# Performance work log

Measured on AMD Instinct MI355X. Metric: run time of the kernel, lower is better.

Reference implementation:

```python
import jax, jax.numpy as jnp
import numpy as np

B, N, D, E, H, F, L = 4096, 32, 128, 256, 8, 1024, 6
DH = E // H  # head dim = 32
LN_EPS = 1e-5


def setup_inputs() -> dict:
    key = jax.random.key(0)
    ks = jax.random.split(key, 8)
    def s(k, shape, fan_in):
        return (jax.random.normal(k, shape, jnp.float32) / np.float32(np.sqrt(fan_in)))
    inp = {
        "obs": jax.random.normal(ks[0], (B, D), jnp.float32),
        "emb_W": s(ks[1], (N, D, E), D),          # per-node tokenizer Linear weights
        "emb_b": jnp.zeros((N, E), jnp.float32),
        "pos_emb": jax.random.normal(ks[2], (N, E), jnp.float32) * 0.02,
        "Wqkv": s(ks[3], (3 * E, E), E),          # shared across all L layers (torch code shares one layer object)
        "bqkv": jnp.zeros((3 * E,), jnp.float32),
        "Wo": s(ks[4], (E, E), E),
        "bo": jnp.zeros((E,), jnp.float32),
        "ln1_g": jnp.ones((E,), jnp.float32),
        "ln1_b": jnp.zeros((E,), jnp.float32),
        "ln2_g": jnp.ones((E,), jnp.float32),
        "ln2_b": jnp.zeros((E,), jnp.float32),
        "W1": s(ks[5], (E, F), E),
        "b1": jnp.zeros((F,), jnp.float32),
        "W2": s(ks[6], (F, E), F),
        "b2": jnp.zeros((E,), jnp.float32),
    }
    # kinematic-chain adjacency (|i-j|<=1) incl. forced self-loops, additive mask
    idx = jnp.arange(N)
    adj = jnp.abs(idx[:, None] - idx[None, :]) <= 1
    inp["adj_mask"] = jnp.where(adj, 0.0, -1e9).astype(jnp.float32)  # [N, N]
    return inp


def _layer_norm(x, g, b):
    m = jnp.mean(x, axis=-1, keepdims=True)
    v = jnp.var(x, axis=-1, keepdims=True)
    return (x - m) * jax.lax.rsqrt(v + LN_EPS) * g + b


def _encoder_layer(x, adj_mask, Wqkv, bqkv, Wo, bo, ln1_g, ln1_b, ln2_g, ln2_b, W1, b1, W2, b2):
    # pre-LN self-attention block
    h = _layer_norm(x, ln1_g, ln1_b)                      # [B, N, E]
    qkv = h @ Wqkv.T + bqkv                               # [B, N, 3E]
    q, k, v = jnp.split(qkv, 3, axis=-1)
    q = q.reshape(B, N, H, DH).transpose(0, 2, 1, 3)      # [B, H, N, DH]
    k = k.reshape(B, N, H, DH).transpose(0, 2, 1, 3)
    v = v.reshape(B, N, H, DH).transpose(0, 2, 1, 3)
    scale = np.float32(1.0 / np.sqrt(DH))
    scores = jnp.einsum('bhqd,bhkd->bhqk', q, k) * scale + adj_mask  # [B, H, N, N]
    attn = jax.nn.softmax(scores, axis=-1)
    o = jnp.einsum('bhqk,bhkd->bhqd', attn, v)
    o = o.transpose(0, 2, 1, 3).reshape(B, N, E)
    x = x + (o @ Wo.T + bo)
    # pre-LN feed-forward block (ReLU)
    h2 = _layer_norm(x, ln2_g, ln2_b)
    x = x + (jax.nn.relu(h2 @ W1 + b1) @ W2 + b2)
    return x


def reference(obs, emb_W, emb_b, pos_emb, Wqkv, bqkv, Wo, bo,
              ln1_g, ln1_b, ln2_g, ln2_b, W1, b1, W2, b2, adj_mask):
    # per-node MLP tokenizer (every node sees full obs): [B,D] x [N,D,E] -> [B,N,E]
    x = jnp.einsum('bd,nde->bne', obs, emb_W) + emb_b + pos_emb
    # BoT-Hard: all L layers masked; torch ModuleList shares a single layer's params
    for _ in range(L):
        x = _encoder_layer(x, adj_mask, Wqkv, bqkv, Wo, bo,
                           ln1_g, ln1_b, ln2_g, ln2_b, W1, b1, W2, b2)
    return x
```

## Files before the change

kernel.cpp:

```cpp
#include <hip/hip_runtime.h>
#include <hip/hip_bf16.h>
#include <stdint.h>

#define B_ 4096
#define N_ 32
#define D_ 128
#define E_ 256
#define H_ 8
#define F_ 1024
#define L_ 6
#define M_ (B_ * N_)

typedef unsigned short u16;
typedef __attribute__((ext_vector_type(8))) short short8;
typedef __attribute__((ext_vector_type(4))) short short4v;
typedef __attribute__((ext_vector_type(4))) float floatx4;

__device__ __forceinline__ float b2f(u16 u) {
  union { unsigned int i; float f; } c;
  c.i = ((unsigned int)u) << 16;
  return c.f;
}
__device__ __forceinline__ u16 f2b(float f) {
  union { float f; unsigned int i; } c;
  c.f = f;
  unsigned int x = c.i;
  return (u16)((x + 0x7fffu + ((x >> 16) & 1u)) >> 16);
}

typedef __attribute__((address_space(1))) void* gas_ptr;
typedef __attribute__((address_space(3))) void* las_ptr;
__device__ __forceinline__ void async16(const u16* g, u16* l) {
  __builtin_amdgcn_global_load_lds((gas_ptr)g, (las_ptr)l, 16, 0, 0);
}

#define RAW_BARRIER() __builtin_amdgcn_s_barrier()
#define WAITV(n) asm volatile("s_waitcnt vmcnt(" #n ")" ::: "memory")

template <bool RELU>
__global__ __launch_bounds__(256) void gemm_async(
    const u16* __restrict__ A, int lda,
    const u16* __restrict__ Bt,
    const float* __restrict__ bias,
    u16* __restrict__ C, int ldc,
    int K) {
  __shared__ u16 As[2][128 * 32];
  __shared__ u16 Bs[2][128 * 32];
  const int tid = threadIdx.x;
  const int wave = tid >> 6;
  const int lane = tid & 63;
  const int wm = wave & 1;
  const int wn = wave >> 1;
  const int lrow = lane & 15;
  const int quad = lane >> 4;
  const long m0 = (long)blockIdx.x * 128;
  const long n0 = (long)blockIdx.y * 128;

  const u16* Ab = A + m0 * lda;
  const u16* Bb = Bt + n0 * K;

  floatx4 acc[4][4];
#pragma unroll
  for (int a = 0; a < 4; ++a)
#pragma unroll
    for (int b = 0; b < 4; ++b) acc[a][b] = floatx4{0.f, 0.f, 0.f, 0.f};

  const int rr = tid >> 2;
  const int oo = (tid & 3) * 8;

#define ISSUE_GA(p, kb)                                              \
  do {                                                               \
    async16(Ab + (long)rr * lda + (kb) + oo, &As[p][wave * 512]);    \
    async16(Ab + (long)(rr + 64) * lda + (kb) + oo,                  \
            &As[p][2048 + wave * 512]);                              \
    async16(Bb + (long)rr * K + (kb) + oo, &Bs[p][wave * 512]);      \
    async16(Bb + (long)(rr + 64) * K + (kb) + oo,                    \
            &Bs[p][2048 + wave * 512]);                              \
  } while (0)

  const int T = K >> 5;
  ISSUE_GA(0, 0);
  for (int i = 0; i < T; ++i) {
    const int cur = i & 1;
    RAW_BARRIER();
    if (i + 1 < T) {
      ISSUE_GA(cur ^ 1, (i + 1) * 32);
      WAITV(4);
    } else {
      WAITV(0);
    }
    RAW_BARRIER();
    short8 af[4], bfr[4];
#pragma unroll
    for (int t = 0; t < 4; ++t) {
      af[t] = *(const short8*)(&As[cur][(wm * 64 + t * 16 + lrow) * 32 + quad * 8]);
      bfr[t] = *(const short8*)(&Bs[cur][(wn * 64 + t * 16 + lrow) * 32 + quad * 8]);
    }
#pragma unroll
    for (int tm = 0; tm < 4; ++tm)
#pragma unroll
      for (int tn = 0; tn < 4; ++tn)
        acc[tm][tn] = __builtin_amdgcn_mfma_f32_16x16x32_bf16(af[tm], bfr[tn], acc[tm][tn], 0, 0, 0);
  }
#undef ISSUE_GA

#pragma unroll
  for (int tn = 0; tn < 4; ++tn) {
    const long col = n0 + wn * 64 + tn * 16 + lrow;
    const float bv = bias[col];
#pragma unroll
    for (int tm = 0; tm < 4; ++tm) {
#pragma unroll
      for (int r = 0; r < 4; ++r) {
        const long row = m0 + wm * 64 + tm * 16 + quad * 4 + r;
        float v = acc[tm][tn][r] + bv;
        if (RELU) v = fmaxf(v, 0.0f);
        C[row * (long)ldc + col] = f2b(v);
      }
    }
  }
}

template <bool RESID>
__global__ __launch_bounds__(512) void gemm_ln(
    const u16* __restrict__ A, int lda, long sAz,
    const u16* __restrict__ Bt, long sBz,
    const float* __restrict__ bias, long sBiasz,
    float* __restrict__ xout, u16* __restrict__ hout,
    int ldc, long sCz,
    const float* __restrict__ resid,
    const float* __restrict__ g, const float* __restrict__ be,
    int K) {
  __shared__ u16 As[2][128 * 32];
  __shared__ u16 Bs[2][256 * 32];
  __shared__ float part[128][4][2];
  const int tid = threadIdx.x;
  const int wave = tid >> 6;
  const int lane = tid & 63;
  const int wm = wave >> 2;
  const int wn = wave & 3;
  const int lrow = lane & 15;
  const int quad = lane >> 4;
  const int z = blockIdx.z;
  const long m0 = (long)blockIdx.x * 128;

  const u16* Ab = A + (long)z * sAz + m0 * lda;
  const u16* Bb = Bt + (long)z * sBz;

  floatx4 acc[4][4];
#pragma unroll
  for (int a = 0; a < 4; ++a)
#pragma unroll
    for (int b = 0; b < 4; ++b) acc[a][b] = floatx4{0.f, 0.f, 0.f, 0.f};

  const int rr = tid >> 2;
  const int oo = (tid & 3) * 8;

#define ISSUE_GL(p, kb)                                               \
  do {                                                                \
    async16(Ab + (long)rr * lda + (kb) + oo, &As[p][wave * 512]);     \
    async16(Bb + (long)rr * K + (kb) + oo, &Bs[p][wave * 512]);       \
    async16(Bb + (long)(rr + 128) * K + (kb) + oo,                    \
            &Bs[p][4096 + wave * 512]);                               \
  } while (0)

  const int T = K >> 5;
  ISSUE_GL(0, 0);
  for (int i = 0; i < T; ++i) {
    const int cur = i & 1;
    RAW_BARRIER();
    if (i + 1 < T) {
      ISSUE_GL(cur ^ 1, (i + 1) * 32);
      WAITV(3);
    } else {
      WAITV(0);
    }
    RAW_BARRIER();
    short8 af[4], bfr[4];
#pragma unroll
    for (int t = 0; t < 4; ++t) {
      af[t] = *(const short8*)(&As[cur][(wm * 64 + t * 16 + lrow) * 32 + quad * 8]);
      bfr[t] = *(const short8*)(&Bs[cur][(wn * 64 + t * 16 + lrow) * 32 + quad * 8]);
    }
#pragma unroll
    for (int tm = 0; tm < 4; ++tm)
#pragma unroll
      for (int tn = 0; tn < 4; ++tn)
        acc[tm][tn] = __builtin_amdgcn_mfma_f32_16x16x32_bf16(af[tm], bfr[tn], acc[tm][tn], 0, 0, 0);
  }
#undef ISSUE_GL

  const long cz = (long)z * sCz;
  float bv[4];
#pragma unroll
  for (int tn = 0; tn < 4; ++tn)
    bv[tn] = bias[(long)z * sBiasz + wn * 64 + tn * 16 + lrow];
#pragma unroll
  for (int tm = 0; tm < 4; ++tm) {
#pragma unroll
    for (int r = 0; r < 4; ++r) {
      const long row = m0 + wm * 64 + tm * 16 + quad * 4 + r;
#pragma unroll
      for (int tn = 0; tn < 4; ++tn) {
        float v = acc[tm][tn][r] + bv[tn];
        if (RESID) {
          const long col = wn * 64 + tn * 16 + lrow;
          v += resid[cz + row * (long)ldc + col];
        }
        acc[tm][tn][r] = v;
      }
    }
  }

#pragma unroll
  for (int tm = 0; tm < 4; ++tm) {
#pragma unroll
    for (int r = 0; r < 4; ++r) {
      float s = acc[tm][0][r] + acc[tm][1][r] + acc[tm][2][r] + acc[tm][3][r];
      float q = acc[tm][0][r] * acc[tm][0][r] + acc[tm][1][r] * acc[tm][1][r] +
                acc[tm][2][r] * acc[tm][2][r] + acc[tm][3][r] * acc[tm][3][r];
#pragma unroll
      for (int mk = 1; mk <= 8; mk <<= 1) {
        s += __shfl_xor(s, mk, 64);
        q += __shfl_xor(q, mk, 64);
      }
      if (lrow == 0) {
        const int lr = wm * 64 + tm * 16 + quad * 4 + r;
        part[lr][wn][0] = s;
        part[lr][wn][1] = q;
      }
    }
  }
  __syncthreads();

  float gv[4], bev[4];
#pragma unroll
  for (int tn = 0; tn < 4; ++tn) {
    const int col = wn * 64 + tn * 16 + lrow;
    gv[tn] = g[col];
    bev[tn] = be[col];
  }
#pragma unroll
  for (int tm = 0; tm < 4; ++tm) {
#pragma unroll
    for (int r = 0; r < 4; ++r) {
      const int lr = wm * 64 + tm * 16 + quad * 4 + r;
      const float s = part[lr][0][0] + part[lr][1][0] + part[lr][2][0] + part[lr][3][0];
      const float q = part[lr][0][1] + part[lr][1][1] + part[lr][2][1] + part[lr][3][1];
      const float mean = s * (1.0f / 256.0f);
      const float var = q * (1.0f / 256.0f) - mean * mean;
      const float rstd = rsqrtf(var + 1e-5f);
      const long row = m0 + lr;
#pragma unroll
      for (int tn = 0; tn < 4; ++tn) {
        const int col = wn * 64 + tn * 16 + lrow;
        const long idx = cz + row * (long)ldc + col;
        const float v = acc[tm][tn][r];
        xout[idx] = v;
        hout[idx] = f2b((v - mean) * rstd * gv[tn] + bev[tn]);
      }
    }
  }
}

__global__ __launch_bounds__(256) void attn_kernel(const u16* __restrict__ qkv,
                                                   u16* __restrict__ o) {
  __shared__ u16 sh[32 * 768];
  const int tid = threadIdx.x;
  const int wave = tid >> 6;
  const int lane = tid & 63;
  const long b = blockIdx.x;
  const u16* src = qkv + b * (32L * 768);

#pragma unroll
  for (int p = 0; p < 12; ++p) {
    const int s = p * 256 + wave * 64 + lane;
    const int row = s / 96;
    const int cir = s - row * 96;
    const int gsl = row * 96 + (cir ^ (row & 7));
    async16(src + (long)gsl * 8, &sh[p * 2048 + wave * 512]);
  }
  WAITV(0);
  __syncthreads();

  const int i = tid & 31;
  const int h = (tid >> 5) & 7;
  const long m = b * 32 + i;

  float q[32];
#pragma unroll
  for (int c = 0; c < 4; ++c) {
    short8 qv = *(const short8*)(&sh[i * 768 + (((h * 4 + c) ^ (i & 7)) << 3)]);
#pragma unroll
    for (int k = 0; k < 8; ++k) q[c * 8 + k] = b2f((u16)qv[k]);
  }
  float sc[3];
  int jc[3];
#pragma unroll
  for (int jj = 0; jj < 3; ++jj) {
    const int j = i - 1 + jj;
    const bool valid = (j >= 0) && (j < 32);
    const int jcl = valid ? j : i;
    jc[jj] = jcl;
    float dot = 0.0f;
#pragma unroll
    for (int c = 0; c < 4; ++c) {
      short8 kv = *(const short8*)(
          &sh[jcl * 768 + ((32 + ((h * 4 + c) ^ (jcl & 7))) << 3)]);
#pragma unroll
      for (int k = 0; k < 8; ++k) dot += q[c * 8 + k] * b2f((u16)kv[k]);
    }
    sc[jj] = valid ? dot * 0.17677669529663687f : -3.0e38f;
  }
  const float mx = fmaxf(sc[0], fmaxf(sc[1], sc[2]));
  const float w0 = __expf(sc[0] - mx);
  const float w1 = __expf(sc[1] - mx);
  const float w2 = __expf(sc[2] - mx);
  const float inv = 1.0f / (w0 + w1 + w2);
  const float w[3] = {w0 * inv, w1 * inv, w2 * inv};
  float acc[32];
#pragma unroll
  for (int k = 0; k < 32; ++k) acc[k] = 0.0f;
#pragma unroll
  for (int jj = 0; jj < 3; ++jj) {
    const int jcl = jc[jj];
    const float wj = w[jj];
#pragma unroll
    for (int c = 0; c < 4; ++c) {
      short8 vv = *(const short8*)(
          &sh[jcl * 768 + ((64 + ((h * 4 + c) ^ (jcl & 7))) << 3)]);
#pragma unroll
      for (int k = 0; k < 8; ++k) acc[c * 8 + k] += wj * b2f((u16)vv[k]);
    }
  }
  u16* op = o + m * 256 + h * 32;
#pragma unroll
  for (int c = 0; c < 4; ++c) {
    short8 ov;
#pragma unroll
    for (int k = 0; k < 8; ++k) ov[k] = (short)f2b(acc[c * 8 + k]);
    *(short8*)(op + c * 8) = ov;
  }
}

__global__ __launch_bounds__(256) void transpose_f2b(const float* __restrict__ src,
                                                     u16* __restrict__ dst,
                                                     int R, int C) {
  const long base = (long)blockIdx.z * R * C;
  const int idx = blockIdx.x * 256 + threadIdx.x;
  if (idx < R * C) {
    const int r = idx / C;
    const int c = idx - r * C;
    dst[base + (long)c * R + r] = f2b(src[base + idx]);
  }
}

__global__ __launch_bounds__(256) void cvt_f2b_kernel(const float* __restrict__ s,
                                                      u16* __restrict__ d, int n) {
  const int i = blockIdx.x * 256 + threadIdx.x;
  if (i < n) d[i] = f2b(s[i]);
}

__global__ __launch_bounds__(256) void addf_kernel(const float* __restrict__ a,
                                                   const float* __restrict__ b,
                                                   float* __restrict__ d, int n) {
  const int i = blockIdx.x * 256 + threadIdx.x;
  if (i < n) d[i] = a[i] + b[i];
}

extern "C" void kernel_launch(void* const* d_in, const int* in_sizes, int n_in,
                              void* d_out, int out_size, void* d_ws, size_t ws_size,
                              hipStream_t stream) {
  (void)in_sizes; (void)n_in; (void)out_size; (void)ws_size;
  const float* obs   = (const float*)d_in[0];
  const float* emb_W = (const float*)d_in[1];
  const float* emb_b = (const float*)d_in[2];
  const float* pos   = (const float*)d_in[3];
  const float* Wqkv  = (const float*)d_in[4];
  const float* bqkv  = (const float*)d_in[5];
  const float* Wo    = (const float*)d_in[6];
  const float* bo    = (const float*)d_in[7];
  const float* ln1_g = (const float*)d_in[8];
  const float* ln1_b = (const float*)d_in[9];
  const float* ln2_g = (const float*)d_in[10];
  const float* ln2_b = (const float*)d_in[11];
  const float* W1    = (const float*)d_in[12];
  const float* b1    = (const float*)d_in[13];
  const float* W2    = (const float*)d_in[14];
  const float* b2    = (const float*)d_in[15];

  float* x = (float*)d_out;

  char* ws = (char*)d_ws;
  u16* hbuf   = (u16*)ws;   ws += (size_t)M_ * E_ * 2;
  u16* sbuf   = (u16*)ws;   ws += (size_t)M_ * F_ * 2;
  u16* embWt  = (u16*)ws;   ws += (size_t)N_ * D_ * E_ * 2;
  u16* obs_bf = (u16*)ws;   ws += (size_t)B_ * D_ * 2;
  u16* wqkv_bf= (u16*)ws;   ws += (size_t)3 * E_ * E_ * 2;
  u16* wo_bf  = (u16*)ws;   ws += (size_t)E_ * E_ * 2;
  u16* w1t    = (u16*)ws;   ws += (size_t)E_ * F_ * 2;
  u16* w2t    = (u16*)ws;   ws += (size_t)E_ * F_ * 2;
  float* cbias= (float*)ws; ws += (size_t)N_ * E_ * 4;

  transpose_f2b<<<dim3((D_ * E_ + 255) / 256, 1, N_), 256, 0, stream>>>(emb_W, embWt, D_, E_);
  transpose_f2b<<<dim3((E_ * F_ + 255) / 256, 1, 1), 256, 0, stream>>>(W1, w1t, E_, F_);
  transpose_f2b<<<dim3((E_ * F_ + 255) / 256, 1, 1), 256, 0, stream>>>(W2, w2t, F_, E_);
  cvt_f2b_kernel<<<(B_ * D_ + 255) / 256, 256, 0, stream>>>(obs, obs_bf, B_ * D_);
  cvt_f2b_kernel<<<(3 * E_ * E_ + 255) / 256, 256, 0, stream>>>(Wqkv, wqkv_bf, 3 * E_ * E_);
  cvt_f2b_kernel<<<(E_ * E_ + 255) / 256, 256, 0, stream>>>(Wo, wo_bf, E_ * E_);
  addf_kernel<<<(N_ * E_ + 255) / 256, 256, 0, stream>>>(emb_b, pos, cbias, N_ * E_);

  gemm_ln<false><<<dim3(B_ / 128, 1, N_), 512, 0, stream>>>(
      obs_bf, D_, 0, embWt, (long)E_ * D_, cbias, E_,
      x, hbuf, N_ * E_, E_, nullptr, ln1_g, ln1_b, D_);

  for (int l = 0; l < L_; ++l) {
    gemm_async<false><<<dim3(M_ / 128, 768 / 128, 1), 256, 0, stream>>>(
        hbuf, E_, wqkv_bf, bqkv, sbuf, 768, E_);
    attn_kernel<<<B_, 256, 0, stream>>>(sbuf, hbuf);
    gemm_ln<true><<<dim3(M_ / 128, 1, 1), 512, 0, stream>>>(
        hbuf, E_, 0, wo_bf, 0, bo, 0,
        x, hbuf, E_, 0, x, ln2_g, ln2_b, E_);
    gemm_async<true><<<dim3(M_ / 128, F_ / 128, 1), 256, 0, stream>>>(
        hbuf, E_, w1t, b1, sbuf, F_, E_);
    gemm_ln<true><<<dim3(M_ / 128, 1, 1), 512, 0, stream>>>(
        sbuf, F_, 0, w2t, 0, b2, 0,
        x, hbuf, E_, 0, x, ln1_g, ln1_b, F_);
  }
}
```

Before: 3.931 ms.

## Fuse all six encoder layers into one persistent per-tile kernel

Replaces the 30 per-layer launches (QKV GEMM, attention, Wo GEMM+LN, FFN1, FFN2+LN) with a single kernel. Each block owns 64 token rows (two batch items) and keeps the residual stream in registers and the activations in LDS for all layers. The FFN is chunked over F so the 1024-wide intermediate never goes to global memory. The aim is to remove the global round trips of the QKV, attention and FFN intermediates plus the launch overhead. In exchange, weight fragments are read straight from global/L2 with no LDS staging, and the large LDS footprint and register use may limit occupancy and MFMA efficiency.

```diff
diff --git a/kernel.cpp b/kernel.cpp
--- a/kernel.cpp
+++ b/kernel.cpp
@@ -36,90 +36,7 @@
 
 #define RAW_BARRIER() __builtin_amdgcn_s_barrier()
 #define WAITV(n) asm volatile("s_waitcnt vmcnt(" #n ")" ::: "memory")
-
-template <bool RELU>
-__global__ __launch_bounds__(256) void gemm_async(
-    const u16* __restrict__ A, int lda,
-    const u16* __restrict__ Bt,
-    const float* __restrict__ bias,
-    u16* __restrict__ C, int ldc,
-    int K) {
-  __shared__ u16 As[2][128 * 32];
-  __shared__ u16 Bs[2][128 * 32];
-  const int tid = threadIdx.x;
-  const int wave = tid >> 6;
-  const int lane = tid & 63;
-  const int wm = wave & 1;
-  const int wn = wave >> 1;
-  const int lrow = lane & 15;
-  const int quad = lane >> 4;
-  const long m0 = (long)blockIdx.x * 128;
-  const long n0 = (long)blockIdx.y * 128;
-
-  const u16* Ab = A + m0 * lda;
-  const u16* Bb = Bt + n0 * K;
-
-  floatx4 acc[4][4];
-#pragma unroll
-  for (int a = 0; a < 4; ++a)
-#pragma unroll
-    for (int b = 0; b < 4; ++b) acc[a][b] = floatx4{0.f, 0.f, 0.f, 0.f};
-
-  const int rr = tid >> 2;
-  const int oo = (tid & 3) * 8;
-
-#define ISSUE_GA(p, kb)                                              \
-  do {                                                               \
-    async16(Ab + (long)rr * lda + (kb) + oo, &As[p][wave * 512]);    \
-    async16(Ab + (long)(rr + 64) * lda + (kb) + oo,                  \
-            &As[p][2048 + wave * 512]);                              \
-    async16(Bb + (long)rr * K + (kb) + oo, &Bs[p][wave * 512]);      \
-    async16(Bb + (long)(rr + 64) * K + (kb) + oo,                    \
-            &Bs[p][2048 + wave * 512]);                              \
-  } while (0)
-
-  const int T = K >> 5;
-  ISSUE_GA(0, 0);
-  for (int i = 0; i < T; ++i) {
-    const int cur = i & 1;
-    RAW_BARRIER();
-    if (i + 1 < T) {
-      ISSUE_GA(cur ^ 1, (i + 1) * 32);
-      WAITV(4);
-    } else {
-      WAITV(0);
-    }
-    RAW_BARRIER();
-    short8 af[4], bfr[4];
-#pragma unroll
-    for (int t = 0; t < 4; ++t) {
-      af[t] = *(const short8*)(&As[cur][(wm * 64 + t * 16 + lrow) * 32 + quad * 8]);
-      bfr[t] = *(const short8*)(&Bs[cur][(wn * 64 + t * 16 + lrow) * 32 + quad * 8]);
-    }
-#pragma unroll
-    for (int tm = 0; tm < 4; ++tm)
-#pragma unroll
-      for (int tn = 0; tn < 4; ++tn)
-        acc[tm][tn] = __builtin_amdgcn_mfma_f32_16x16x32_bf16(af[tm], bfr[tn], acc[tm][tn], 0, 0, 0);
-  }
-#undef ISSUE_GA
-
-#pragma unroll
-  for (int tn = 0; tn < 4; ++tn) {
-    const long col = n0 + wn * 64 + tn * 16 + lrow;
-    const float bv = bias[col];
-#pragma unroll
-    for (int tm = 0; tm < 4; ++tm) {
-#pragma unroll
-      for (int r = 0; r < 4; ++r) {
-        const long row = m0 + wm * 64 + tm * 16 + quad * 4 + r;
-        float v = acc[tm][tn][r] + bv;
-        if (RELU) v = fmaxf(v, 0.0f);
-        C[row * (long)ldc + col] = f2b(v);
-      }
-    }
-  }
-}
+#define MFMA16(a, b, c) __builtin_amdgcn_mfma_f32_16x16x32_bf16(a, b, c, 0, 0, 0)
 
 template <bool RESID>
 __global__ __launch_bounds__(512) void gemm_ln(
@@ -186,7 +103,7 @@
     for (int tm = 0; tm < 4; ++tm)
 #pragma unroll
       for (int tn = 0; tn < 4; ++tn)
-        acc[tm][tn] = __builtin_amdgcn_mfma_f32_16x16x32_bf16(af[tm], bfr[tn], acc[tm][tn], 0, 0, 0);
+        acc[tm][tn] = MFMA16(af[tm], bfr[tn], acc[tm][tn]);
   }
 #undef ISSUE_GL
 
@@ -263,84 +180,294 @@
   }
 }
 
-__global__ __launch_bounds__(256) void attn_kernel(const u16* __restrict__ qkv,
-                                                   u16* __restrict__ o) {
-  __shared__ u16 sh[32 * 768];
+__device__ __forceinline__ void ln_write_h(
+    floatx4 (&xr)[2][4], u16* hsm, float (*part)[4][2],
+    const int (&mrow)[2], int wn, int quad, int msw,
+    const float* __restrict__ g, const float* __restrict__ b) {
+  float s0 = 0.f, q0 = 0.f, s1 = 0.f, q1 = 0.f;
+#pragma unroll
+  for (int ni = 0; ni < 4; ++ni)
+#pragma unroll
+    for (int r = 0; r < 4; ++r) {
+      const float v0 = xr[0][ni][r], v1 = xr[1][ni][r];
+      s0 += v0; q0 += v0 * v0; s1 += v1; q1 += v1 * v1;
+    }
+  s0 += __shfl_xor(s0, 16, 64); s0 += __shfl_xor(s0, 32, 64);
+  q0 += __shfl_xor(q0, 16, 64); q0 += __shfl_xor(q0, 32, 64);
+  s1 += __shfl_xor(s1, 16, 64); s1 += __shfl_xor(s1, 32, 64);
+  q1 += __shfl_xor(q1, 16, 64); q1 += __shfl_xor(q1, 32, 64);
+  if (quad == 0) {
+    part[mrow[0]][wn][0] = s0; part[mrow[0]][wn][1] = q0;
+    part[mrow[1]][wn][0] = s1; part[mrow[1]][wn][1] = q1;
+  }
+  __syncthreads();
+#pragma unroll
+  for (int mi = 0; mi < 2; ++mi) {
+    const float S = part[mrow[mi]][0][0] + part[mrow[mi]][1][0] +
+                    part[mrow[mi]][2][0] + part[mrow[mi]][3][0];
+    const float Q = part[mrow[mi]][0][1] + part[mrow[mi]][1][1] +
+                    part[mrow[mi]][2][1] + part[mrow[mi]][3][1];
+    const float mean = S * (1.0f / 256.0f);
+    const float rstd = rsqrtf(Q * (1.0f / 256.0f) - mean * mean + 1e-5f);
+#pragma unroll
+    for (int ni = 0; ni < 4; ++ni) {
+      const int n0 = wn * 64 + ni * 16 + quad * 4;
+      const floatx4 gg = *(const floatx4*)(g + n0);
+      const floatx4 bb = *(const floatx4*)(b + n0);
+      short4v ov;
+#pragma unroll
+      for (int r = 0; r < 4; ++r)
+        ov[r] = (short)f2b((xr[mi][ni][r] - mean) * rstd * gg[r] + bb[r]);
+      *(short4v*)(&hsm[mrow[mi] * 256 + (((n0 >> 3) ^ msw) << 3) + (n0 & 7)]) = ov;
+    }
+  }
+  __syncthreads();
+}
+
+__global__ __launch_bounds__(512, 2) void layers_kernel(
+    float* __restrict__ x,
+    const u16* __restrict__ hbuf,
+    const u16* __restrict__ wq,
+    const u16* __restrict__ wo,
+    const u16* __restrict__ w1t,
+    const u16* __restrict__ w2t,
+    const float* __restrict__ bqkv, const float* __restrict__ bo,
+    const float* __restrict__ b1, const float* __restrict__ b2,
+    const float* __restrict__ ln1g, const float* __restrict__ ln1b,
+    const float* __restrict__ ln2g, const float* __restrict__ ln2b) {
+  __shared__ u16 hsm[64 * 256];
+  __shared__ u16 scr[64 * 768];
+  __shared__ float part[64][4][2];
+
   const int tid = threadIdx.x;
   const int wave = tid >> 6;
   const int lane = tid & 63;
-  const long b = blockIdx.x;
-  const u16* src = qkv + b * (32L * 768);
-
-#pragma unroll
-  for (int p = 0; p < 12; ++p) {
-    const int s = p * 256 + wave * 64 + lane;
-    const int row = s / 96;
-    const int cir = s - row * 96;
-    const int gsl = row * 96 + (cir ^ (row & 7));
-    async16(src + (long)gsl * 8, &sh[p * 2048 + wave * 512]);
-  }
-  WAITV(0);
+  const int wm = wave >> 2;
+  const int wn = wave & 3;
+  const int lrow = lane & 15;
+  const int quad = lane >> 4;
+  const int msw = lrow & 7;
+  const long row0 = (long)blockIdx.x * 64;
+
+  const int mrow[2] = {wm * 32 + lrow, wm * 32 + 16 + lrow};
+  const int hb0 = mrow[0] * 256;
+  const int hb1 = mrow[1] * 256;
+  const int ncol0 = wn * 64 + quad * 4;
+
+  floatx4 xr[2][4];
+#pragma unroll
+  for (int mi = 0; mi < 2; ++mi)
+#pragma unroll
+    for (int ni = 0; ni < 4; ++ni)
+      xr[mi][ni] = *(const floatx4*)(x + (row0 + mrow[mi]) * 256 + ncol0 + ni * 16);
+
+#pragma unroll
+  for (int it = 0; it < 4; ++it) {
+    const int sl = it * 512 + tid;
+    const int m = sl >> 5;
+    const int s = sl & 31;
+    short8 v = *(const short8*)(hbuf + (row0 + m) * 256 + s * 8);
+    *(short8*)(&hsm[m * 256 + ((s ^ (m & 7)) << 3)]) = v;
+  }
   __syncthreads();
 
-  const int i = tid & 31;
-  const int h = (tid >> 5) & 7;
-  const long m = b * 32 + i;
-
-  float q[32];
-#pragma unroll
-  for (int c = 0; c < 4; ++c) {
-    short8 qv = *(const short8*)(&sh[i * 768 + (((h * 4 + c) ^ (i & 7)) << 3)]);
-#pragma unroll
-    for (int k = 0; k < 8; ++k) q[c * 8 + k] = b2f((u16)qv[k]);
-  }
-  float sc[3];
-  int jc[3];
-#pragma unroll
-  for (int jj = 0; jj < 3; ++jj) {
-    const int j = i - 1 + jj;
-    const bool valid = (j >= 0) && (j < 32);
-    const int jcl = valid ? j : i;
-    jc[jj] = jcl;
-    float dot = 0.0f;
-#pragma unroll
-    for (int c = 0; c < 4; ++c) {
-      short8 kv = *(const short8*)(
-          &sh[jcl * 768 + ((32 + ((h * 4 + c) ^ (jcl & 7))) << 3)]);
-#pragma unroll
-      for (int k = 0; k < 8; ++k) dot += q[c * 8 + k] * b2f((u16)kv[k]);
-    }
-    sc[jj] = valid ? dot * 0.17677669529663687f : -3.0e38f;
-  }
-  const float mx = fmaxf(sc[0], fmaxf(sc[1], sc[2]));
-  const float w0 = __expf(sc[0] - mx);
-  const float w1 = __expf(sc[1] - mx);
-  const float w2 = __expf(sc[2] - mx);
-  const float inv = 1.0f / (w0 + w1 + w2);
-  const float w[3] = {w0 * inv, w1 * inv, w2 * inv};
-  float acc[32];
-#pragma unroll
-  for (int k = 0; k < 32; ++k) acc[k] = 0.0f;
-#pragma unroll
-  for (int jj = 0; jj < 3; ++jj) {
-    const int jcl = jc[jj];
-    const float wj = w[jj];
-#pragma unroll
-    for (int c = 0; c < 4; ++c) {
-      short8 vv = *(const short8*)(
-          &sh[jcl * 768 + ((64 + ((h * 4 + c) ^ (jcl & 7))) << 3)]);
-#pragma unroll
-      for (int k = 0; k < 8; ++k) acc[c * 8 + k] += wj * b2f((u16)vv[k]);
-    }
-  }
-  u16* op = o + m * 256 + h * 32;
-#pragma unroll
-  for (int c = 0; c < 4; ++c) {
-    short8 ov;
-#pragma unroll
-    for (int k = 0; k < 8; ++k) ov[k] = (short)f2b(acc[c * 8 + k]);
-    *(short8*)(op + c * 8) = ov;
-  }
+  for (int l = 0; l < L_; ++l) {
+    {
+      floatx4 qa[2][12];
+#pragma unroll
+      for (int mi = 0; mi < 2; ++mi)
+#pragma unroll
+        for (int ni = 0; ni < 12; ++ni) qa[mi][ni] = floatx4{0.f, 0.f, 0.f, 0.f};
+      const u16* wqb = wq + (wn * 192 + lrow) * 256 + quad * 8;
+#pragma unroll
+      for (int ks = 0; ks < 8; ++ks) {
+        const int hoff = (((ks * 4 + quad) ^ msw) << 3);
+        const short8 bf0 = *(const short8*)(&hsm[hb0 + hoff]);
+        const short8 bf1 = *(const short8*)(&hsm[hb1 + hoff]);
+#pragma unroll
+        for (int ni = 0; ni < 12; ++ni) {
+          const short8 af = *(const short8*)(wqb + ni * 16 * 256 + ks * 32);
+          qa[0][ni] = MFMA16(af, bf0, qa[0][ni]);
+          qa[1][ni] = MFMA16(af, bf1, qa[1][ni]);
+        }
+      }
+#pragma unroll
+      for (int mi = 0; mi < 2; ++mi)
+#pragma unroll
+        for (int ni = 0; ni < 12; ++ni) {
+          const int n0 = wn * 192 + ni * 16 + quad * 4;
+          const floatx4 bv = *(const floatx4*)(bqkv + n0);
+          short4v ov;
+#pragma unroll
+          for (int r = 0; r < 4; ++r) ov[r] = (short)f2b(qa[mi][ni][r] + bv[r]);
+          *(short4v*)(&scr[mrow[mi] * 768 + (((n0 >> 3) ^ msw) << 3) + (n0 & 7)]) = ov;
+        }
+    }
+    __syncthreads();
+
+    {
+      const int bl = tid >> 8;
+      const int ii = tid & 31;
+      const int hh = (tid >> 5) & 7;
+      const int am = bl * 32 + ii;
+      const int hs = hh * 4;
+      float q[32];
+#pragma unroll
+      for (int c = 0; c < 4; ++c) {
+        const short8 qv = *(const short8*)(&scr[am * 768 + (((hs + c) ^ (am & 7)) << 3)]);
+#pragma unroll
+        for (int k = 0; k < 8; ++k) q[c * 8 + k] = b2f((u16)qv[k]);
+      }
+      float sc[3];
+      int jcv[3];
+#pragma unroll
+      for (int jj = 0; jj < 3; ++jj) {
+        const int j = ii - 1 + jj;
+        const bool valid = (j >= 0) && (j < 32);
+        const int jc = valid ? j : ii;
+        jcv[jj] = jc;
+        const int jm = bl * 32 + jc;
+        float dot = 0.0f;
+#pragma unroll
+        for (int c = 0; c < 4; ++c) {
+          const short8 kv = *(const short8*)(
+              &scr[jm * 768 + ((32 + ((hs + c) ^ (jm & 7))) << 3)]);
+#pragma unroll
+          for (int k = 0; k < 8; ++k) dot += q[c * 8 + k] * b2f((u16)kv[k]);
+        }
+        sc[jj] = valid ? dot * 0.17677669529663687f : -3.0e38f;
+      }
+      const float mx = fmaxf(sc[0], fmaxf(sc[1], sc[2]));
+      const float w0 = __expf(sc[0] - mx);
+      const float w1 = __expf(sc[1] - mx);
+      const float w2 = __expf(sc[2] - mx);
+      const float inv = 1.0f / (w0 + w1 + w2);
+      const float w[3] = {w0 * inv, w1 * inv, w2 * inv};
+      float oa[32];
+#pragma unroll
+      for (int k = 0; k < 32; ++k) oa[k] = 0.0f;
+#pragma unroll
+      for (int jj = 0; jj < 3; ++jj) {
+        const int jm = bl * 32 + jcv[jj];
+        const float wj = w[jj];
+#pragma unroll
+        for (int c = 0; c < 4; ++c) {
+          const short8 vv = *(const short8*)(
+              &scr[jm * 768 + ((64 + ((hs + c) ^ (jm & 7))) << 3)]);
+#pragma unroll
+          for (int k = 0; k < 8; ++k) oa[c * 8 + k] += wj * b2f((u16)vv[k]);
+        }
+      }
+#pragma unroll
+      for (int c = 0; c < 4; ++c) {
+        short8 ov;
+#pragma unroll
+        for (int k = 0; k < 8; ++k) ov[k] = (short)f2b(oa[c * 8 + k]);
+        *(short8*)(&hsm[am * 256 + (((hs + c) ^ (am & 7)) << 3)]) = ov;
+      }
+    }
+    __syncthreads();
+
+    {
+      floatx4 pa[2][4];
+#pragma unroll
+      for (int mi = 0; mi < 2; ++mi)
+#pragma unroll
+        for (int ni = 0; ni < 4; ++ni) pa[mi][ni] = floatx4{0.f, 0.f, 0.f, 0.f};
+      const u16* wob = wo + (wn * 64 + lrow) * 256 + quad * 8;
+#pragma unroll
+      for (int ks = 0; ks < 8; ++ks) {
+        const int hoff = (((ks * 4 + quad) ^ msw) << 3);
+        const short8 bf0 = *(const short8*)(&hsm[hb0 + hoff]);
+        const short8 bf1 = *(const short8*)(&hsm[hb1 + hoff]);
+#pragma unroll
+        for (int ni = 0; ni < 4; ++ni) {
+          const short8 af = *(const short8*)(wob + ni * 16 * 256 + ks * 32);
+          pa[0][ni] = MFMA16(af, bf0, pa[0][ni]);
+          pa[1][ni] = MFMA16(af, bf1, pa[1][ni]);
+        }
+      }
+#pragma unroll
+      for (int mi = 0; mi < 2; ++mi)
+#pragma unroll
+        for (int ni = 0; ni < 4; ++ni) {
+          const floatx4 bv = *(const floatx4*)(bo + wn * 64 + ni * 16 + quad * 4);
+          xr[mi][ni] = xr[mi][ni] + pa[mi][ni] + bv;
+        }
+    }
+    ln_write_h(xr, hsm, part, mrow, wn, quad, msw, ln2g, ln2b);
+
+    {
+      floatx4 fa[2][4];
+#pragma unroll
+      for (int mi = 0; mi < 2; ++mi)
+#pragma unroll
+        for (int ni = 0; ni < 4; ++ni) fa[mi][ni] = floatx4{0.f, 0.f, 0.f, 0.f};
+      for (int fc = 0; fc < 4; ++fc) {
+        floatx4 ga[2][4];
+#pragma unroll
+        for (int mi = 0; mi < 2; ++mi)
+#pragma unroll
+          for (int ni = 0; ni < 4; ++ni) ga[mi][ni] = floatx4{0.f, 0.f, 0.f, 0.f};
+        const u16* w1b = w1t + (fc * 256 + wn * 64 + lrow) * 256 + quad * 8;
+#pragma unroll
+        for (int ks = 0; ks < 8; ++ks) {
+          const int hoff = (((ks * 4 + quad) ^ msw) << 3);
+          const short8 bf0 = *(const short8*)(&hsm[hb0 + hoff]);
+          const short8 bf1 = *(const short8*)(&hsm[hb1 + hoff]);
+#pragma unroll
+          for (int ni = 0; ni < 4; ++ni) {
+            const short8 af = *(const short8*)(w1b + ni * 16 * 256 + ks * 32);
+            ga[0][ni] = MFMA16(af, bf0, ga[0][ni]);
+            ga[1][ni] = MFMA16(af, bf1, ga[1][ni]);
+          }
+        }
+#pragma unroll
+        for (int mi = 0; mi < 2; ++mi)
+#pragma unroll
+          for (int ni = 0; ni < 4; ++ni) {
+            const int n0 = wn * 64 + ni * 16 + quad * 4;
+            const floatx4 bv = *(const floatx4*)(b1 + fc * 256 + n0);
+            short4v ov;
+#pragma unroll
+            for (int r = 0; r < 4; ++r)
+              ov[r] = (short)f2b(fmaxf(ga[mi][ni][r] + bv[r], 0.0f));
+            *(short4v*)(&scr[mrow[mi] * 256 + (((n0 >> 3) ^ msw) << 3) + (n0 & 7)]) = ov;
+          }
+        __syncthreads();
+        const u16* w2b = w2t + (wn * 64 + lrow) * 1024 + fc * 256 + quad * 8;
+#pragma unroll
+        for (int ks = 0; ks < 8; ++ks) {
+          const int aoff = (((ks * 4 + quad) ^ msw) << 3);
+          const short8 bf0 = *(const short8*)(&scr[hb0 + aoff]);
+          const short8 bf1 = *(const short8*)(&scr[hb1 + aoff]);
+#pragma unroll
+          for (int ni = 0; ni < 4; ++ni) {
+            const short8 af = *(const short8*)(w2b + ni * 16 * 1024 + ks * 32);
+            fa[0][ni] = MFMA16(af, bf0, fa[0][ni]);
+            fa[1][ni] = MFMA16(af, bf1, fa[1][ni]);
+          }
+        }
+        __syncthreads();
+      }
+#pragma unroll
+      for (int mi = 0; mi < 2; ++mi)
+#pragma unroll
+        for (int ni = 0; ni < 4; ++ni) {
+          const floatx4 bv = *(const floatx4*)(b2 + wn * 64 + ni * 16 + quad * 4);
+          xr[mi][ni] = xr[mi][ni] + fa[mi][ni] + bv;
+        }
+    }
+    if (l < L_ - 1) {
+      ln_write_h(xr, hsm, part, mrow, wn, quad, msw, ln1g, ln1b);
+    }
+  }
+
+#pragma unroll
+  for (int mi = 0; mi < 2; ++mi)
+#pragma unroll
+    for (int ni = 0; ni < 4; ++ni)
+      *(floatx4*)(x + (row0 + mrow[mi]) * 256 + ncol0 + ni * 16) = xr[mi][ni];
 }
 
 __global__ __launch_bounds__(256) void transpose_f2b(const float* __restrict__ src,
@@ -393,7 +520,6 @@
 
   char* ws = (char*)d_ws;
   u16* hbuf   = (u16*)ws;   ws += (size_t)M_ * E_ * 2;
-  u16* sbuf   = (u16*)ws;   ws += (size_t)M_ * F_ * 2;
   u16* embWt  = (u16*)ws;   ws += (size_t)N_ * D_ * E_ * 2;
   u16* obs_bf = (u16*)ws;   ws += (size_t)B_ * D_ * 2;
   u16* wqkv_bf= (u16*)ws;   ws += (size_t)3 * E_ * E_ * 2;
@@ -414,17 +540,7 @@
       obs_bf, D_, 0, embWt, (long)E_ * D_, cbias, E_,
       x, hbuf, N_ * E_, E_, nullptr, ln1_g, ln1_b, D_);
 
-  for (int l = 0; l < L_; ++l) {
-    gemm_async<false><<<dim3(M_ / 128, 768 / 128, 1), 256, 0, stream>>>(
-        hbuf, E_, wqkv_bf, bqkv, sbuf, 768, E_);
-    attn_kernel<<<B_, 256, 0, stream>>>(sbuf, hbuf);
-    gemm_ln<true><<<dim3(M_ / 128, 1, 1), 512, 0, stream>>>(
-        hbuf, E_, 0, wo_bf, 0, bo, 0,
-        x, hbuf, E_, 0, x, ln2_g, ln2_b, E_);
-    gemm_async<true><<<dim3(M_ / 128, F_ / 128, 1), 256, 0, stream>>>(
-        hbuf, E_, w1t, b1, sbuf, F_, E_);
-    gemm_ln<true><<<dim3(M_ / 128, 1, 1), 512, 0, stream>>>(
-        sbuf, F_, 0, w2t, 0, b2, 0,
-        x, hbuf, E_, 0, x, ln1_g, ln1_b, F_);
-  }
-}
+  layers_kernel<<<B_ / 2, 512, 0, stream>>>(
+      x, hbuf, wqkv_bf, wo_bf, w1t, w2t,
+      bqkv, bo, b1, b2, ln1_g, ln1_b, ln2_g, ln2_b);
+}
```

Result: slower. 9.327 ms (+137.2%).
